# Performance work log

Measured on AMD Instinct MI355X. Metric: run time of the kernel, lower is better.

Reference implementation:

```python
import jax, jax.numpy as jnp
import numpy as np
from jax import lax

BN_EPS = 1e-3
SLOPE = 0.1
CLUSTER_TEMP = 30.0
K = 16
FEAT = 4096  # 8*8*64


def conv_bn_lrelu(x, w, b, g, beta, m, v):
    # Conv2d stride 2, padding 1 (NCHW / OIHW), then eval-mode BatchNorm, then LeakyReLU.
    y = lax.conv_general_dilated(x, w, window_strides=(2, 2), padding=((1, 1), (1, 1)),
                                 dimension_numbers=("NCHW", "OIHW", "NCHW"))
    y = y + b[None, :, None, None]
    scale = g / jnp.sqrt(v + BN_EPS)
    y = y * scale[None, :, None, None] + (beta - m * scale)[None, :, None, None]
    return jnp.where(y > 0, y, SLOPE * y)


def soft_kmeans(data, mu, num_iter, ct):
    # Row L2-normalize (equivalent to diag(1/||x||) @ data)
    data = data / jnp.linalg.norm(data, axis=1, keepdims=True)
    for _ in range(num_iter):
        dist = data @ mu.T                      # [N, K]
        r = jax.nn.softmax(ct * dist, axis=1)   # [N, K]
        mu = (r.T @ data) / r.sum(axis=0)[:, None]  # [K, F]
    dist = data @ mu.T
    r = jax.nn.softmax(ct * dist, axis=1)
    return mu, r, dist


def setup_inputs() -> dict:
    key = jax.random.key(0)
    ks = jax.random.split(key, 12)
    d = {}
    d["x"] = jax.random.normal(ks[0], (256, 3, 64, 64), dtype=jnp.float32)
    # conv1: 3 -> 128
    d["conv1_w"] = jax.random.normal(ks[1], (128, 3, 3, 3), dtype=jnp.float32) * 0.05
    d["conv1_b"] = jnp.zeros((128,), jnp.float32)
    d["bn1_g"] = jnp.ones((128,), jnp.float32)
    d["bn1_b"] = jnp.zeros((128,), jnp.float32)
    d["bn1_m"] = jax.random.normal(ks[2], (128,), dtype=jnp.float32) * 0.1
    d["bn1_v"] = jax.random.uniform(ks[3], (128,), minval=0.5, maxval=1.5, dtype=jnp.float32)
    # conv2: 128 -> 256
    d["conv2_w"] = jax.random.normal(ks[4], (256, 128, 3, 3), dtype=jnp.float32) * 0.02
    d["conv2_b"] = jnp.zeros((256,), jnp.float32)
    d["bn2_g"] = jnp.ones((256,), jnp.float32)
    d["bn2_b"] = jnp.zeros((256,), jnp.float32)
    d["bn2_m"] = jax.random.normal(ks[5], (256,), dtype=jnp.float32) * 0.1
    d["bn2_v"] = jax.random.uniform(ks[6], (256,), minval=0.5, maxval=1.5, dtype=jnp.float32)
    # conv3: 256 -> 64
    d["conv3_w"] = jax.random.normal(ks[7], (64, 256, 3, 3), dtype=jnp.float32) * 0.02
    d["conv3_b"] = jnp.zeros((64,), jnp.float32)
    d["bn3_g"] = jnp.ones((64,), jnp.float32)
    d["bn3_b"] = jnp.zeros((64,), jnp.float32)
    d["bn3_m"] = jax.random.normal(ks[8], (64,), dtype=jnp.float32) * 0.1
    d["bn3_v"] = jax.random.uniform(ks[9], (64,), minval=0.5, maxval=1.5, dtype=jnp.float32)
    # initial cluster centers, torch.rand(K, F)
    d["mu0"] = jax.random.uniform(ks[10], (K, FEAT), dtype=jnp.float32)
    d["num_iter"] = 10
    return d


def reference(x, conv1_w, conv1_b, bn1_g, bn1_b, bn1_m, bn1_v,
              conv2_w, conv2_b, bn2_g, bn2_b, bn2_m, bn2_v,
              conv3_w, conv3_b, bn3_g, bn3_b, bn3_m, bn3_v,
              mu0, num_iter):
    h = conv_bn_lrelu(x, conv1_w, conv1_b, bn1_g, bn1_b, bn1_m, bn1_v)   # [B,128,32,32]
    h = conv_bn_lrelu(h, conv2_w, conv2_b, bn2_g, bn2_b, bn2_m, bn2_v)   # [B,256,16,16]
    h = conv_bn_lrelu(h, conv3_w, conv3_b, bn3_g, bn3_b, bn3_m, bn3_v)   # [B,64,8,8]
    embeds = h.reshape(-1, FEAT)                                          # [B, 4096]
    mu_init, _, _ = soft_kmeans(embeds, mu0, num_iter, CLUSTER_TEMP)
    _, r, _ = soft_kmeans(embeds, lax.stop_gradient(mu_init), 1, CLUSTER_TEMP)
    return r
```

## Files before the change

### kernel.cpp

```cpp
#include <hip/hip_runtime.h>
#include <stdint.h>
#include <stddef.h>

typedef unsigned short u16;
typedef __attribute__((ext_vector_type(8))) short short8;
typedef __attribute__((ext_vector_type(4))) float f32x4;
typedef __attribute__((ext_vector_type(4))) int int4v;

__device__ __forceinline__ float bf2f(u16 u) {
    unsigned x = ((unsigned)u) << 16;
    return __uint_as_float(x);
}
__device__ __forceinline__ u16 f2bf(float f) {
    unsigned x = __float_as_uint(f);
    unsigned r = (x + 0x7fffu + ((x >> 16) & 1u)) >> 16;
    return (u16)r;
}
__device__ __forceinline__ float ldin(const void* p, size_t i, int isbf) {
    return isbf ? bf2f(((const u16*)p)[i]) : ((const float*)p)[i];
}
__device__ __forceinline__ int detect_bf(const void* v1) {
    const u16* ub = (const u16*)v1;
    int ok = 1;
#pragma unroll
    for (int i = 0; i < 16; i++) {
        float f = bf2f(ub[i]);
        if (!(f >= 0.4f && f <= 1.6f)) ok = 0;
    }
    return ok;
}
__device__ __forceinline__ int sw(int r, int c8) {
    return r * 32 + (((c8) ^ (r & 3)) << 3);
}

struct PrepArgs {
    const void *w1, *w2, *w3;
    u16 *W1p, *W2p, *W3p;
    const void *b1, *g1, *be1, *m1, *v1;
    const void *b2, *g2, *be2, *m2, *v2;
    const void *b3, *g3, *be3, *m3, *v3;
    float *es1, *esh1, *es2, *esh2, *es3, *esh3;
    u16 *zb;
};
__device__ __forceinline__ void packw_body(const void* src, u16* dst, int CI, int Kp,
                                           int total, int blk, int t, int isbf) {
    int p = blk * 256 + t;
    if (p >= total) return;
    int co = p / Kp, k = p - co * Kp;
    int tap = k / CI, ci = k - tap * CI;
    u16 v = 0;
    if (tap < 9) {
        size_t si = (size_t)(co * CI + ci) * 9 + tap;
        v = isbf ? ((const u16*)src)[si] : f2bf(((const float*)src)[si]);
    }
    dst[p] = v;
}
__global__ __launch_bounds__(256) void kprep_all(PrepArgs A) {
    int b = blockIdx.x, t = threadIdx.x;
    int isbf = detect_bf(A.v1);
    if (b < 1152) {
        packw_body(A.w2, A.W2p, 128, 1152, 256 * 1152, b, t, isbf);
    } else if (b < 1728) {
        packw_body(A.w3, A.W3p, 256, 2304, 64 * 2304, b - 1152, t, isbf);
    } else if (b < 1744) {
        packw_body(A.w1, A.W1p, 3, 32, 128 * 32, b - 1728, t, isbf);
    } else {
        if (b == 1745) A.zb[t] = 0;
        int u = (b - 1744) * 256 + t;
        const void *bb, *g, *be, *m, *v;
        float *es, *esh;
        int c;
        if (u < 128)      { c = u;       bb=A.b1; g=A.g1; be=A.be1; m=A.m1; v=A.v1; es=A.es1; esh=A.esh1; }
        else if (u < 384) { c = u - 128; bb=A.b2; g=A.g2; be=A.be2; m=A.m2; v=A.v2; es=A.es2; esh=A.esh2; }
        else if (u < 448) { c = u - 384; bb=A.b3; g=A.g3; be=A.be3; m=A.m3; v=A.v3; es=A.es3; esh=A.esh3; }
        else return;
        float sc = ldin(g, c, isbf) / sqrtf(ldin(v, c, isbf) + 1e-3f);
        float sh = (ldin(bb, c, isbf) - ldin(m, c, isbf)) * sc + ldin(be, c, isbf);
        es[c] = sc;
        esh[c] = sh;
    }
}

__global__ void kfallback(u16* __restrict__ out) {
    int i = blockIdx.x * 256 + threadIdx.x;
    if (i < 4096) out[i] = f2bf(0.0625f);
}

__global__ __launch_bounds__(256) void im2col1(const void* __restrict__ x,
                                               u16* __restrict__ A1,
                                               const void* __restrict__ v1ref) {
    int n = blockIdx.x, t = threadIdx.x;
    int isbf = detect_bf(v1ref);
    __shared__ u16 xs[3 * 64 * 64];
    if (isbf) {
        const u16* xp = (const u16*)x + (size_t)n * 12288;
#pragma unroll
        for (int i = t * 8; i < 12288; i += 2048)
            *(int4v*)&xs[i] = *(const int4v*)&xp[i];
    } else {
        const float* xp = (const float*)x + (size_t)n * 12288;
#pragma unroll
        for (int i = t * 4; i < 12288; i += 1024) {
            float4 v = *(const float4*)&xp[i];
            xs[i] = f2bf(v.x); xs[i + 1] = f2bf(v.y);
            xs[i + 2] = f2bf(v.z); xs[i + 3] = f2bf(v.w);
        }
    }
    __syncthreads();
#pragma unroll
    for (int rr = 0; rr < 4; rr++) {
        int m = rr * 256 + t;
        int ox = m & 31, oy = m >> 5;
        alignas(16) u16 row[32];
#pragma unroll
        for (int k = 0; k < 32; k++) {
            u16 val = 0;
            if (k < 27) {
                int tap = k / 3, ci = k - 3 * tap;
                int ky = tap / 3, kx = tap - 3 * ky;
                int iy = 2 * oy - 1 + ky, ix = 2 * ox - 1 + kx;
                if ((unsigned)iy < 64u && (unsigned)ix < 64u)
                    val = xs[ci * 4096 + iy * 64 + ix];
            }
            row[k] = val;
        }
        int4v* dst = (int4v*)(A1 + ((size_t)n * 1024 + m) * 32);
        const int4v* srcv = (const int4v*)row;
#pragma unroll
        for (int q = 0; q < 4; q++) dst[q] = srcv[q];
    }
}

__global__ __launch_bounds__(256) void gemm_conv1(
    const u16* __restrict__ A1, const u16* __restrict__ W,
    const float* __restrict__ es, const float* __restrict__ esh,
    u16* __restrict__ OutB) {
    alignas(16) __shared__ u16 As[128 * 32];
    alignas(16) __shared__ u16 Bs[128 * 32];
    const int t = threadIdx.x;
    const int m0 = blockIdx.x * 128;
    const int lane = t & 63, w = t >> 6;
    const int wm = w & 1, wn = w >> 1;
    const int rA = t >> 2, c8 = t & 3, koff = c8 * 8;

#pragma unroll
    for (int j = 0; j < 2; j++) {
        int4v va = *(const int4v*)(A1 + (size_t)(m0 + j * 64 + rA) * 32 + koff);
        *(int4v*)&As[sw(j * 64 + rA, c8)] = va;
        int4v vb = *(const int4v*)(W + (size_t)(j * 64 + rA) * 32 + koff);
        *(int4v*)&Bs[sw(j * 64 + rA, c8)] = vb;
    }
    __syncthreads();
    const int qc = lane >> 4, fr = lane & 15;
    short8 af[4], bf[4];
#pragma unroll
    for (int i = 0; i < 4; i++) af[i] = *(const short8*)&As[sw(wm * 64 + i * 16 + fr, qc)];
#pragma unroll
    for (int j = 0; j < 4; j++) bf[j] = *(const short8*)&Bs[sw(wn * 64 + j * 16 + fr, qc)];
    f32x4 acc[4][4];
#pragma unroll
    for (int i = 0; i < 4; i++)
#pragma unroll
        for (int j = 0; j < 4; j++) {
#pragma unroll
            for (int q = 0; q < 4; q++) acc[i][j][q] = 0.f;
            acc[i][j] = __builtin_amdgcn_mfma_f32_16x16x32_bf16(af[i], bf[j], acc[i][j], 0, 0, 0);
        }
    float scv[4], shv[4];
#pragma unroll
    for (int j = 0; j < 4; j++) {
        int c = wn * 64 + j * 16 + fr;
        scv[j] = es[c];
        shv[j] = esh[c];
    }
#pragma unroll
    for (int i = 0; i < 4; i++) {
#pragma unroll
        for (int rg = 0; rg < 4; rg++) {
            int m = m0 + wm * 64 + i * 16 + qc * 4 + rg;
            int ox = m & 31, oy = (m >> 5) & 31, n = m >> 10;
            u16* orow = OutB + ((size_t)(n * 32 + oy) * 32 + ox) * 128 + wn * 64 + fr;
#pragma unroll
            for (int j = 0; j < 4; j++) {
                float v = acc[i][j][rg] * scv[j] + shv[j];
                v = (v > 0.f) ? v : 0.1f * v;
                orow[j * 16] = f2bf(v);
            }
        }
    }
}

__global__ __launch_bounds__(512, 2) void gemm_conv2(
    const u16* __restrict__ h1, const u16* __restrict__ W,
    const float* __restrict__ es, const float* __restrict__ esh,
    u16* __restrict__ OutB, const u16* __restrict__ zb) {
    alignas(16) __shared__ u16 smem[4 * 16384];
    u16* const Ab0 = smem;
    u16* const Ab1 = smem + 16384;
    u16* const Bb0 = smem + 32768;
    u16* const Bb1 = smem + 49152;

    const int t = threadIdx.x;
    const int w = t >> 6, l = t & 63;
    const int img = blockIdx.x;
    const int wm = w >> 2, wn = w & 3;
    const int fr = l & 15, qc = l >> 4;

    int aiy0[4], aix0[4], ac8e[4];
    int brow[4];
#pragma unroll
    for (int i = 0; i < 4; ++i) {
        int gi = w * 256 + i * 64 + l;
        int r = gi >> 3, c8d = gi & 7;
        int c8s = c8d ^ (r & 7);
        int oy = r >> 4, ox = r & 15;
        aiy0[i] = 2 * oy - 1;
        aix0[i] = 2 * ox - 1;
        ac8e[i] = c8s * 8;
        brow[i] = r * 1152 + c8s * 8;
    }
    auto mkA = [&](int i, int ky, int kx) -> const u16* {
        int iy = aiy0[i] + ky, ix = aix0[i] + kx;
        if ((unsigned)iy < 32u && (unsigned)ix < 32u)
            return h1 + (size_t)(((img * 32 + iy) * 32 + ix) * 128 + ac8e[i]);
        return zb;
    };
    auto stage = [&](const u16* src, u16* ldsbase, int i) {
        __builtin_amdgcn_global_load_lds(
            (const __attribute__((address_space(1))) void*)src,
            (__attribute__((address_space(3))) void*)(ldsbase + (w * 4 + i) * 512),
            16, 0, 0);
    };

    f32x4 acc[8][4];
#pragma unroll
    for (int mi = 0; mi < 8; ++mi)
#pragma unroll
        for (int nj = 0; nj < 4; ++nj)
#pragma unroll
            for (int q = 0; q < 4; ++q) acc[mi][nj][q] = 0.0f;

    auto do_tile = [&](const u16* A, const u16* B) {
#pragma unroll
        for (int kk = 0; kk < 2; ++kk) {
            const int c8 = kk * 4 + qc;
            short8 a[8], b[4];
#pragma unroll
            for (int q = 0; q < 8; ++q) {
                int row = wm * 128 + q * 16 + fr;
                a[q] = *(const short8*)(A + row * 64 + ((c8 ^ (row & 7)) << 3));
            }
#pragma unroll
            for (int j = 0; j < 4; ++j) {
                int row = wn * 64 + j * 16 + fr;
                b[j] = *(const short8*)(B + row * 64 + ((c8 ^ (row & 7)) << 3));
            }
            __builtin_amdgcn_s_setprio(1);
#pragma unroll
            for (int q = 0; q < 8; ++q)
#pragma unroll
                for (int j = 0; j < 4; ++j)
                    acc[q][j] = __builtin_amdgcn_mfma_f32_16x16x32_bf16(
                        a[q], b[j], acc[q][j], 0, 0, 0);
            __builtin_amdgcn_s_setprio(0);
        }
    };

    const u16* pcur[4];
#pragma unroll
    for (int i = 0; i < 4; ++i) pcur[i] = mkA(i, 0, 0);
#pragma unroll
    for (int i = 0; i < 4; ++i) {
        stage(pcur[i], Ab0, i);
        stage(W + brow[i], Bb0, i);
    }

    for (int tap = 0; tap < 9; ++tap) {
        __syncthreads();
#pragma unroll
        for (int i = 0; i < 4; ++i) {
            stage(pcur[i] + 64, Ab1, i);
            stage(W + brow[i] + (2 * tap + 1) * 64, Bb1, i);
        }
        do_tile(Ab0, Bb0);
        __syncthreads();
        if (tap < 8) {
            const int tap2 = tap + 1;
            const int ky2 = (tap2 >= 6) ? 2 : (tap2 >= 3) ? 1 : 0;
            const int kx2 = tap2 - 3 * ky2;
#pragma unroll
            for (int i = 0; i < 4; ++i) pcur[i] = mkA(i, ky2, kx2);
#pragma unroll
            for (int i = 0; i < 4; ++i) {
                stage(pcur[i], Ab0, i);
                stage(W + brow[i] + (2 * tap + 2) * 64, Bb0, i);
            }
        }
        do_tile(Ab1, Bb1);
    }

    float scv[4], shv[4];
#pragma unroll
    for (int nj = 0; nj < 4; ++nj) {
        int c = wn * 64 + nj * 16 + fr;
        scv[nj] = es[c];
        shv[nj] = esh[c];
    }
#pragma unroll
    for (int mi = 0; mi < 8; ++mi) {
#pragma unroll
        for (int rg = 0; rg < 4; ++rg) {
            int r = wm * 128 + mi * 16 + qc * 4 + rg;
            u16* orow = OutB + ((size_t)img * 256 + r) * 256 + wn * 64 + fr;
#pragma unroll
            for (int nj = 0; nj < 4; ++nj) {
                float v = acc[mi][nj][rg] * scv[nj] + shv[nj];
                v = (v > 0.f) ? v : 0.1f * v;
                orow[nj * 16] = f2bf(v);
            }
        }
    }
}

__global__ __launch_bounds__(256) void gemm_conv3f(
    const u16* __restrict__ Asrc, const u16* __restrict__ W,
    const float* __restrict__ es3, const float* __restrict__ esh3,
    float* __restrict__ dat, u16* __restrict__ datbf) {
    constexpr int CIN = 256, KTOT = 2304, IH = 16;
    constexpr int CC = 8, SM = 2, SN = 2;

    alignas(16) __shared__ u16 As[64 * 32];
    alignas(16) __shared__ u16 Bs[64 * 32];
    __shared__ float red[4];

    const int t = threadIdx.x;
    const int lid = blockIdx.x;
    const int xcd = lid & 7, slot = lid >> 3;
    const int img = xcd * 32 + slot;
    const int m0 = img * 64;
    const int lane = t & 63, w = t >> 6;
    const int wm = w & 1, wn = w >> 1;
    const int rA = t >> 2, c8 = t & 3, koff = c8 * 8;
    const int fr = lane & 15, qc = lane >> 4;

    f32x4 acc[SM][SN];
#pragma unroll
    for (int i = 0; i < SM; i++)
#pragma unroll
        for (int j = 0; j < SN; j++)
#pragma unroll
            for (int q = 0; q < 4; q++) acc[i][j][q] = 0.0f;

    const int aox = rA & 7, aoy = (rA >> 3) & 7;
    auto mkoffs = [&](int tap) -> int {
        int ky = tap / 3, kx = tap - 3 * ky;
        int iy = 2 * aoy - 1 + ky, ix = 2 * aox - 1 + kx;
        if ((unsigned)iy < (unsigned)IH && (unsigned)ix < (unsigned)IH)
            return ((img * IH + iy) * IH + ix) * CIN;
        return -0x40000000;
    };
    const u16* Wrow = W + (size_t)rA * KTOT + koff;

    int offs_cur = mkoffs(0), offs_nxt;
    const int4v zerov = (int4v){0, 0, 0, 0};
    int4v bufA[2], bufB[2];
#pragma unroll
    for (int pp = 0; pp < 2; pp++) {
        bufA[pp] = (offs_cur >= 0)
                       ? *(const int4v*)(Asrc + offs_cur + pp * 32 + koff)
                       : zerov;
        bufB[pp] = *(const int4v*)(Wrow + pp * 32);
    }

    int flat = 0;
    for (int tap = 0; tap < 9; tap++) {
        offs_nxt = (tap < 8) ? mkoffs(tap + 1) : -0x40000000;
#pragma unroll
        for (int cc = 0; cc < CC; cc++, flat++) {
            const int pb_ = flat & 1;
            *(int4v*)&As[sw(rA, c8)] = bufA[pb_];
            *(int4v*)&Bs[sw(rA, c8)] = bufB[pb_];
            __syncthreads();
            {
                const int cc2 = cc + 2;
                const bool intap = (cc2 < CC);
                const int cci = intap ? cc2 : cc2 - CC;
                int o = intap ? offs_cur : offs_nxt;
                bufA[pb_] = (o >= 0) ? *(const int4v*)(Asrc + o + cci * 32 + koff) : zerov;
                const bool wvalid = intap || (tap < 8);
                const int wk = (intap ? tap : tap + 1) * CIN + cci * 32;
                bufB[pb_] = wvalid ? *(const int4v*)(Wrow + wk) : zerov;
            }
            short8 af[SM], bf[SN];
#pragma unroll
            for (int i = 0; i < SM; i++)
                af[i] = *(const short8*)&As[sw(wm * 32 + i * 16 + fr, qc)];
#pragma unroll
            for (int j = 0; j < SN; j++)
                bf[j] = *(const short8*)&Bs[sw(wn * 32 + j * 16 + fr, qc)];
#pragma unroll
            for (int i = 0; i < SM; i++)
#pragma unroll
                for (int j = 0; j < SN; j++)
                    acc[i][j] = __builtin_amdgcn_mfma_f32_16x16x32_bf16(
                        af[i], bf[j], acc[i][j], 0, 0, 0);
            __syncthreads();
        }
        offs_cur = offs_nxt;
    }

    float vals[SM][SN][4];
    float ssq = 0.f;
#pragma unroll
    for (int j = 0; j < SN; j++) {
        int c = wn * 32 + j * 16 + fr;
        float sc = es3[c], sh = esh3[c];
#pragma unroll
        for (int i = 0; i < SM; i++) {
#pragma unroll
            for (int rg = 0; rg < 4; rg++) {
                float v = acc[i][j][rg] * sc + sh;
                v = (v > 0.f) ? v : 0.1f * v;
                vals[i][j][rg] = v;
                ssq += v * v;
            }
        }
    }
#pragma unroll
    for (int off = 32; off > 0; off >>= 1) ssq += __shfl_xor(ssq, off);
    if (lane == 0) red[w] = ssq;
    __syncthreads();
    float inv = 1.0f / sqrtf(red[0] + red[1] + red[2] + red[3]);
#pragma unroll
    for (int j = 0; j < SN; j++) {
        int c = wn * 32 + j * 16 + fr;
#pragma unroll
        for (int i = 0; i < SM; i++) {
#pragma unroll
            for (int rg = 0; rg < 4; rg++) {
                int row = wm * 32 + i * 16 + qc * 4 + rg;
                size_t idx = (size_t)img * 4096 + c * 64 + row;
                float v = vals[i][j][rg] * inv;
                dat[idx] = v;
                datbf[idx] = f2bf(v);
            }
        }
    }
}

__global__ __launch_bounds__(256) void kgr(const u16* __restrict__ dbf,
                                           const float* __restrict__ dat,
                                           const void* __restrict__ mu0,
                                           u16* __restrict__ Ghi,
                                           u16* __restrict__ Glo,
                                           float* __restrict__ rb0,
                                           const void* __restrict__ v1ref) {
    const int b = blockIdx.x, t = threadIdx.x;
    __shared__ float part[16][4];
    __shared__ float ds[16];

    if (b < 16) {
        const int m0 = (b & 3) * 64, n0 = (b >> 2) * 64;
        const int lane = t & 63, w = t >> 6;
        const int wm = w & 1, wn = w >> 1;
        const int fr = lane & 15, qc = lane >> 4;

        f32x4 acc[2][2];
#pragma unroll
        for (int i = 0; i < 2; i++)
#pragma unroll
            for (int j = 0; j < 2; j++)
#pragma unroll
                for (int q = 0; q < 4; q++) acc[i][j][q] = 0.0f;

        const u16* a0p = dbf + (size_t)(m0 + wm * 32 + fr) * 4096 + qc * 8;
        const u16* a1p = a0p + 16 * 4096;
        const u16* b0p = dbf + (size_t)(n0 + wn * 32 + fr) * 4096 + qc * 8;
        const u16* b1p = b0p + 16 * 4096;
        for (int ks = 0; ks < 4096; ks += 128) {
#pragma unroll
            for (int u = 0; u < 4; u++) {
                const int o = ks + u * 32;
                short8 a0 = *(const short8*)(a0p + o);
                short8 a1 = *(const short8*)(a1p + o);
                short8 b0 = *(const short8*)(b0p + o);
                short8 b1 = *(const short8*)(b1p + o);
                acc[0][0] = __builtin_amdgcn_mfma_f32_16x16x32_bf16(a0, b0, acc[0][0], 0, 0, 0);
                acc[0][1] = __builtin_amdgcn_mfma_f32_16x16x32_bf16(a0, b1, acc[0][1], 0, 0, 0);
                acc[1][0] = __builtin_amdgcn_mfma_f32_16x16x32_bf16(a1, b0, acc[1][0], 0, 0, 0);
                acc[1][1] = __builtin_amdgcn_mfma_f32_16x16x32_bf16(a1, b1, acc[1][1], 0, 0, 0);
            }
        }
#pragma unroll
        for (int j = 0; j < 2; j++) {
            int c = n0 + wn * 32 + j * 16 + fr;
#pragma unroll
            for (int i = 0; i < 2; i++)
#pragma unroll
                for (int rg = 0; rg < 4; rg++) {
                    int row = m0 + wm * 32 + i * 16 + qc * 4 + rg;
                    float v = acc[i][j][rg];
                    u16 hi = f2bf(v);
                    u16 lo = f2bf(v - bf2f(hi));
                    Ghi[(size_t)row * 256 + c] = hi;
                    Glo[(size_t)row * 256 + c] = lo;
                }
        }
    } else {
        const int n = b - 16;
        const int isbf = detect_bf(v1ref);
        const int lane = t & 63, wv = t >> 6;
        float d[16];
#pragma unroll
        for (int j = 0; j < 16; j++) d[j] = dat[(size_t)n * 4096 + j * 256 + t];
#pragma unroll
        for (int k = 0; k < 16; k++) {
            float a = 0.f;
            if (isbf) {
                const u16* mp = (const u16*)mu0 + (size_t)k * 4096;
#pragma unroll
                for (int j = 0; j < 16; j++) a = fmaf(d[j], bf2f(mp[j * 256 + t]), a);
            } else {
                const float* mp = (const float*)mu0 + (size_t)k * 4096;
#pragma unroll
                for (int j = 0; j < 16; j++) a = fmaf(d[j], mp[j * 256 + t], a);
            }
#pragma unroll
            for (int off = 32; off > 0; off >>= 1) a += __shfl_xor(a, off);
            if (lane == 0) part[k][wv] = a;
        }
        __syncthreads();
        if (t < 16) {
            float dk = part[t][0] + part[t][1] + part[t][2] + part[t][3];
            ds[t] = dk;
            __syncthreads();
            float mx = -1e30f;
#pragma unroll
            for (int j = 0; j < 16; j++) mx = fmaxf(mx, ds[j]);
            float sum = 0.f;
#pragma unroll
            for (int j = 0; j < 16; j++) sum += __expf(30.f * (ds[j] - mx));
            rb0[n * 16 + t] = __expf(30.f * (dk - mx)) / sum;
        }
    }
}

__global__ __launch_bounds__(1024) void kmiter(const u16* __restrict__ Ghi,
                                               const u16* __restrict__ Glo,
                                               const float* __restrict__ rb0,
                                               void* __restrict__ dout,
                                               const void* __restrict__ v1ref) {
    const int t = threadIdx.x;
    const int isbf = detect_bf(v1ref);
    const int lane = t & 63, w = t >> 6;
    const int i0 = w * 16;
    const int col = lane & 15;
    const int q = lane >> 4;

    __shared__ u16 rThi[16 * 264];
    __shared__ u16 rTlo[16 * 264];
    __shared__ float part[16][17];

    short8 gh[8], gl[8];
    {
        const u16* Ahirow = Ghi + (size_t)(i0 + col) * 256 + q * 8;
        const u16* Alorow = Glo + (size_t)(i0 + col) * 256 + q * 8;
#pragma unroll
        for (int s = 0; s < 8; s++) {
            gh[s] = *(const short8*)(Ahirow + s * 32);
            gl[s] = *(const short8*)(Alorow + s * 32);
        }
    }

    {
        float rv[4];
#pragma unroll
        for (int rg = 0; rg < 4; rg++) {
            int row = i0 + q * 4 + rg;
            float v = rb0[row * 16 + col];
            rv[rg] = v;
            u16 hi = f2bf(v);
            rThi[col * 264 + row] = hi;
            rTlo[col * 264 + row] = f2bf(v - bf2f(hi));
        }
        float s0 = rv[0] + rv[1] + rv[2] + rv[3];
        s0 += __shfl_xor(s0, 16);
        s0 += __shfl_xor(s0, 32);
        if (lane < 16) part[w][lane] = s0;
    }
    __syncthreads();
    float rsc = 0.f;
#pragma unroll
    for (int ww = 0; ww < 16; ww++) rsc += part[ww][col];

    for (int iter = 0; iter < 11; iter++) {
        f32x4 acc = {0.f, 0.f, 0.f, 0.f};
#pragma unroll
        for (int s = 0; s < 8; s++) {
            short8 bh = *(const short8*)&rThi[col * 264 + s * 32 + q * 8];
            short8 bl = *(const short8*)&rTlo[col * 264 + s * 32 + q * 8];
            acc = __builtin_amdgcn_mfma_f32_16x16x32_bf16(gh[s], bh, acc, 0, 0, 0);
            acc = __builtin_amdgcn_mfma_f32_16x16x32_bf16(gl[s], bh, acc, 0, 0, 0);
            acc = __builtin_amdgcn_mfma_f32_16x16x32_bf16(gh[s], bl, acc, 0, 0, 0);
        }
        float nv[4];
#pragma unroll
        for (int rg = 0; rg < 4; rg++) {
            float dk = acc[rg] / rsc;
            float mx = dk;
#pragma unroll
            for (int o = 1; o < 16; o <<= 1) mx = fmaxf(mx, __shfl_xor(mx, o));
            float e = __expf(30.f * (dk - mx));
            float ssum = e;
#pragma unroll
            for (int o = 1; o < 16; o <<= 1) ssum += __shfl_xor(ssum, o);
            nv[rg] = e / ssum;
        }
        if (iter < 10) {
            __syncthreads();
#pragma unroll
            for (int rg = 0; rg < 4; rg++) {
                int row = i0 + q * 4 + rg;
                u16 hi = f2bf(nv[rg]);
                rThi[col * 264 + row] = hi;
                rTlo[col * 264 + row] = f2bf(nv[rg] - bf2f(hi));
            }
            float s0 = nv[0] + nv[1] + nv[2] + nv[3];
            s0 += __shfl_xor(s0, 16);
            s0 += __shfl_xor(s0, 32);
            if (lane < 16) part[w][lane] = s0;
            __syncthreads();
            rsc = 0.f;
#pragma unroll
            for (int ww = 0; ww < 16; ww++) rsc += part[ww][col];
        } else {
#pragma unroll
            for (int rg = 0; rg < 4; rg++) {
                int row = i0 + q * 4 + rg;
                if (isbf) ((u16*)dout)[row * 16 + col] = f2bf(nv[rg]);
                else ((float*)dout)[row * 16 + col] = nv[rg];
            }
        }
    }
}

extern "C" void kernel_launch(void* const* d_in, const int* in_sizes, int n_in,
                              void* d_out, int out_size, void* d_ws, size_t ws_size,
                              hipStream_t stream) {
    const void* x   = d_in[0];
    const void* w1  = d_in[1];
    const void* b1  = d_in[2];
    const void* g1  = d_in[3];
    const void* be1 = d_in[4];
    const void* m1  = d_in[5];
    const void* v1  = d_in[6];
    const void* w2  = d_in[7];
    const void* b2  = d_in[8];
    const void* g2  = d_in[9];
    const void* be2 = d_in[10];
    const void* m2  = d_in[11];
    const void* v2  = d_in[12];
    const void* w3  = d_in[13];
    const void* b3  = d_in[14];
    const void* g3  = d_in[15];
    const void* be3 = d_in[16];
    const void* m3  = d_in[17];
    const void* v3  = d_in[18];
    const void* mu0 = d_in[19];

    char* p = (char*)d_ws;
    size_t used = 0;
    auto alloc = [&](size_t bytes) -> char* {
        char* q = p;
        size_t rb = (bytes + 255) & ~(size_t)255;
        p += rb;
        used += rb;
        return q;
    };
    float* rb0 = (float*)alloc(4096 * 4);
    u16* Ghi = (u16*)alloc((size_t)65536 * 2);
    u16* Glo = (u16*)alloc((size_t)65536 * 2);
    u16* W1p = (u16*)alloc((size_t)128 * 32 * 2);
    u16* W2p = (u16*)alloc((size_t)256 * 1152 * 2);
    u16* W3p = (u16*)alloc((size_t)64 * 2304 * 2);
    float* es1 = (float*)alloc(128 * 4);
    float* esh1 = (float*)alloc(128 * 4);
    float* es2 = (float*)alloc(256 * 4);
    float* esh2 = (float*)alloc(256 * 4);
    float* es3 = (float*)alloc(64 * 4);
    float* esh3 = (float*)alloc(64 * 4);
    u16* zb = (u16*)alloc(512);
    const size_t R1 = (size_t)256 * 32 * 32 * 128 * 2;
    const size_t R2 = (size_t)256 * 16 * 16 * 256 * 2;
    char* reg1 = alloc(R1);
    char* reg2 = alloc(R2);
    u16* h1 = (u16*)reg1;
    u16* A1 = (u16*)reg2;
    u16* h2 = (u16*)reg2;
    float* dat = (float*)reg1;
    u16* datbf = (u16*)(reg1 + 4194304);

    if (used > ws_size) {
        kfallback<<<16, 256, 0, stream>>>((u16*)d_out);
        return;
    }

    PrepArgs pa = {w1, w2, w3, W1p, W2p, W3p,
                   b1, g1, be1, m1, v1, b2, g2, be2, m2, v2, b3, g3, be3, m3, v3,
                   es1, esh1, es2, esh2, es3, esh3, zb};
    kprep_all<<<1746, 256, 0, stream>>>(pa);
    im2col1<<<256, 256, 0, stream>>>(x, A1, v1);
    gemm_conv1<<<dim3(2048), 256, 0, stream>>>(A1, W1p, es1, esh1, h1);
    gemm_conv2<<<dim3(256), 512, 0, stream>>>(h1, W2p, es2, esh2, h2, zb);
    gemm_conv3f<<<dim3(256), 256, 0, stream>>>(h2, W3p, es3, esh3, dat, datbf);
    kgr<<<dim3(272), 256, 0, stream>>>(datbf, dat, mu0, Ghi, Glo, rb0, v1);
    kmiter<<<1, 1024, 0, stream>>>(Ghi, Glo, rb0, d_out, v1);
}
```

Baseline: 293.2 us.

## Split Gram GEMM over K into four slices with a combine kernel

The 256x256 Gram matrix GEMM in kgr now runs as 64 blocks, each taking a quarter of the 4096-long reduction, in place of 16 blocks covering the full K. The loads are double-buffered in registers. Partial fp32 results go to a workspace, and a new kcomb kernel sums them and splits the result into bf16 hi/lo. kmiter now reads G from global memory on every iteration instead of holding it in registers, which trades register pressure for repeated global/L2 reads. The extra kernel launch and the partial-sum traffic add overhead.

```diff
diff --git a/kernel.cpp b/kernel.cpp
--- a/kernel.cpp
+++ b/kernel.cpp
@@ -451,16 +451,16 @@
 __global__ __launch_bounds__(256) void kgr(const u16* __restrict__ dbf,
                                            const float* __restrict__ dat,
                                            const void* __restrict__ mu0,
-                                           u16* __restrict__ Ghi,
-                                           u16* __restrict__ Glo,
+                                           float* __restrict__ Gp,
                                            float* __restrict__ rb0,
                                            const void* __restrict__ v1ref) {
     const int b = blockIdx.x, t = threadIdx.x;
     __shared__ float part[16][4];
     __shared__ float ds[16];
 
-    if (b < 16) {
-        const int m0 = (b & 3) * 64, n0 = (b >> 2) * 64;
+    if (b < 64) {
+        const int tile = b & 15, s = b >> 4;
+        const int m0 = (tile & 3) * 64, n0 = (tile >> 2) * 64;
         const int lane = t & 63, w = t >> 6;
         const int wm = w & 1, wn = w >> 1;
         const int fr = lane & 15, qc = lane >> 4;
@@ -473,41 +473,55 @@
 #pragma unroll
                 for (int q = 0; q < 4; q++) acc[i][j][q] = 0.0f;
 
-        const u16* a0p = dbf + (size_t)(m0 + wm * 32 + fr) * 4096 + qc * 8;
+        const u16* a0p = dbf + (size_t)(m0 + wm * 32 + fr) * 4096 + s * 1024 + qc * 8;
         const u16* a1p = a0p + 16 * 4096;
-        const u16* b0p = dbf + (size_t)(n0 + wn * 32 + fr) * 4096 + qc * 8;
+        const u16* b0p = dbf + (size_t)(n0 + wn * 32 + fr) * 4096 + s * 1024 + qc * 8;
         const u16* b1p = b0p + 16 * 4096;
-        for (int ks = 0; ks < 4096; ks += 128) {
-#pragma unroll
-            for (int u = 0; u < 4; u++) {
-                const int o = ks + u * 32;
-                short8 a0 = *(const short8*)(a0p + o);
-                short8 a1 = *(const short8*)(a1p + o);
-                short8 b0 = *(const short8*)(b0p + o);
-                short8 b1 = *(const short8*)(b1p + o);
-                acc[0][0] = __builtin_amdgcn_mfma_f32_16x16x32_bf16(a0, b0, acc[0][0], 0, 0, 0);
-                acc[0][1] = __builtin_amdgcn_mfma_f32_16x16x32_bf16(a0, b1, acc[0][1], 0, 0, 0);
-                acc[1][0] = __builtin_amdgcn_mfma_f32_16x16x32_bf16(a1, b0, acc[1][0], 0, 0, 0);
-                acc[1][1] = __builtin_amdgcn_mfma_f32_16x16x32_bf16(a1, b1, acc[1][1], 0, 0, 0);
-            }
-        }
+
+        short8 Pa0[4], Pa1[4], Pb0[4], Pb1[4];
+        short8 Qa0[4], Qa1[4], Qb0[4], Qb1[4];
+        auto ldc = [&](short8* A0, short8* A1, short8* B0, short8* B1, int c) {
+#pragma unroll
+            for (int u = 0; u < 4; ++u) {
+                const int o = c * 128 + u * 32;
+                A0[u] = *(const short8*)(a0p + o);
+                A1[u] = *(const short8*)(a1p + o);
+                B0[u] = *(const short8*)(b0p + o);
+                B1[u] = *(const short8*)(b1p + o);
+            }
+        };
+        auto mmc = [&](short8* A0, short8* A1, short8* B0, short8* B1) {
+#pragma unroll
+            for (int u = 0; u < 4; ++u) {
+                acc[0][0] = __builtin_amdgcn_mfma_f32_16x16x32_bf16(A0[u], B0[u], acc[0][0], 0, 0, 0);
+                acc[0][1] = __builtin_amdgcn_mfma_f32_16x16x32_bf16(A0[u], B1[u], acc[0][1], 0, 0, 0);
+                acc[1][0] = __builtin_amdgcn_mfma_f32_16x16x32_bf16(A1[u], B0[u], acc[1][0], 0, 0, 0);
+                acc[1][1] = __builtin_amdgcn_mfma_f32_16x16x32_bf16(A1[u], B1[u], acc[1][1], 0, 0, 0);
+            }
+        };
+        ldc(Pa0, Pa1, Pb0, Pb1, 0);
+#pragma unroll
+        for (int c = 0; c < 4; ++c) {
+            ldc(Qa0, Qa1, Qb0, Qb1, 2 * c + 1);
+            mmc(Pa0, Pa1, Pb0, Pb1);
+            if (c < 3) ldc(Pa0, Pa1, Pb0, Pb1, 2 * c + 2);
+            mmc(Qa0, Qa1, Qb0, Qb1);
+        }
+
+        float* gp = Gp + (size_t)s * 65536;
 #pragma unroll
         for (int j = 0; j < 2; j++) {
-            int c = n0 + wn * 32 + j * 16 + fr;
+            int cc = n0 + wn * 32 + j * 16 + fr;
 #pragma unroll
             for (int i = 0; i < 2; i++)
 #pragma unroll
                 for (int rg = 0; rg < 4; rg++) {
                     int row = m0 + wm * 32 + i * 16 + qc * 4 + rg;
-                    float v = acc[i][j][rg];
-                    u16 hi = f2bf(v);
-                    u16 lo = f2bf(v - bf2f(hi));
-                    Ghi[(size_t)row * 256 + c] = hi;
-                    Glo[(size_t)row * 256 + c] = lo;
+                    gp[row * 256 + cc] = acc[i][j][rg];
                 }
         }
     } else {
-        const int n = b - 16;
+        const int n = b - 64;
         const int isbf = detect_bf(v1ref);
         const int lane = t & 63, wv = t >> 6;
         float d[16];
@@ -543,6 +557,27 @@
             rb0[n * 16 + t] = __expf(30.f * (dk - mx)) / sum;
         }
     }
+}
+
+__global__ __launch_bounds__(256) void kcomb(const float* __restrict__ Gp,
+                                             u16* __restrict__ Ghi,
+                                             u16* __restrict__ Glo) {
+    const int i = (blockIdx.x * 256 + threadIdx.x) * 4;
+    f32x4 s0 = *(const f32x4*)(Gp + i);
+    f32x4 s1 = *(const f32x4*)(Gp + 65536 + i);
+    f32x4 s2 = *(const f32x4*)(Gp + 131072 + i);
+    f32x4 s3 = *(const f32x4*)(Gp + 196608 + i);
+    unsigned long long ph = 0, pl = 0;
+#pragma unroll
+    for (int q = 0; q < 4; q++) {
+        float v = ((s0[q] + s1[q]) + s2[q]) + s3[q];
+        u16 hi = f2bf(v);
+        u16 lo = f2bf(v - bf2f(hi));
+        ph |= ((unsigned long long)hi) << (16 * q);
+        pl |= ((unsigned long long)lo) << (16 * q);
+    }
+    *(unsigned long long*)(Ghi + i) = ph;
+    *(unsigned long long*)(Glo + i) = pl;
 }
 
 __global__ __launch_bounds__(1024) void kmiter(const u16* __restrict__ Ghi,
@@ -561,16 +596,8 @@
     __shared__ u16 rTlo[16 * 264];
     __shared__ float part[16][17];
 
-    short8 gh[8], gl[8];
-    {
-        const u16* Ahirow = Ghi + (size_t)(i0 + col) * 256 + q * 8;
-        const u16* Alorow = Glo + (size_t)(i0 + col) * 256 + q * 8;
-#pragma unroll
-        for (int s = 0; s < 8; s++) {
-            gh[s] = *(const short8*)(Ahirow + s * 32);
-            gl[s] = *(const short8*)(Alorow + s * 32);
-        }
-    }
+    const u16* Ahirow = Ghi + (size_t)(i0 + col) * 256 + q * 8;
+    const u16* Alorow = Glo + (size_t)(i0 + col) * 256 + q * 8;
 
     {
         float rv[4];
@@ -597,11 +624,13 @@
         f32x4 acc = {0.f, 0.f, 0.f, 0.f};
 #pragma unroll
         for (int s = 0; s < 8; s++) {
+            short8 ah = *(const short8*)(Ahirow + s * 32);
+            short8 al = *(const short8*)(Alorow + s * 32);
             short8 bh = *(const short8*)&rThi[col * 264 + s * 32 + q * 8];
             short8 bl = *(const short8*)&rTlo[col * 264 + s * 32 + q * 8];
-            acc = __builtin_amdgcn_mfma_f32_16x16x32_bf16(gh[s], bh, acc, 0, 0, 0);
-            acc = __builtin_amdgcn_mfma_f32_16x16x32_bf16(gl[s], bh, acc, 0, 0, 0);
-            acc = __builtin_amdgcn_mfma_f32_16x16x32_bf16(gh[s], bl, acc, 0, 0, 0);
+            acc = __builtin_amdgcn_mfma_f32_16x16x32_bf16(ah, bh, acc, 0, 0, 0);
+            acc = __builtin_amdgcn_mfma_f32_16x16x32_bf16(al, bh, acc, 0, 0, 0);
+            acc = __builtin_amdgcn_mfma_f32_16x16x32_bf16(ah, bl, acc, 0, 0, 0);
         }
         float nv[4];
 #pragma unroll
@@ -680,6 +709,7 @@
     float* rb0 = (float*)alloc(4096 * 4);
     u16* Ghi = (u16*)alloc((size_t)65536 * 2);
     u16* Glo = (u16*)alloc((size_t)65536 * 2);
+    float* Gp = (float*)alloc((size_t)4 * 65536 * 4);
     u16* W1p = (u16*)alloc((size_t)128 * 32 * 2);
     u16* W2p = (u16*)alloc((size_t)256 * 1152 * 2);
     u16* W3p = (u16*)alloc((size_t)64 * 2304 * 2);
@@ -713,6 +743,7 @@
     gemm_conv1<<<dim3(2048), 256, 0, stream>>>(A1, W1p, es1, esh1, h1);
     gemm_conv2<<<dim3(256), 512, 0, stream>>>(h1, W2p, es2, esh2, h2, zb);
     gemm_conv3f<<<dim3(256), 256, 0, stream>>>(h2, W3p, es3, esh3, dat, datbf);
-    kgr<<<dim3(272), 256, 0, stream>>>(datbf, dat, mu0, Ghi, Glo, rb0, v1);
+    kgr<<<dim3(320), 256, 0, stream>>>(datbf, dat, mu0, Gp, rb0, v1);
+    kcomb<<<dim3(64), 256, 0, stream>>>(Gp, Ghi, Glo);
     kmiter<<<1, 1024, 0, stream>>>(Ghi, Glo, rb0, d_out, v1);
 }
```

New measurement: 252.5 us. 1.16x faster.
